# Optimization experiments

Measured on AMD Instinct MI355X. Metric: run time of the kernel, lower is better.

The kernel has to match this reference:

```python
import jax, jax.numpy as jnp
import numpy as np

B, T, D = 64, 4096, 512

def setup_inputs() -> dict:
    key = jax.random.key(0)
    k1, k2 = jax.random.split(key)
    encoder_outputs = jax.random.normal(k1, (B, T, D), dtype=jnp.float32)
    attn_weights_param = jax.random.normal(k2, (D, 1), dtype=jnp.float32)
    return {"encoder_outputs": encoder_outputs, "attn_weights_param": attn_weights_param}

def reference(encoder_outputs, attn_weights_param):
    # scores: [B, T] = encoder_outputs @ v  (GEMV per batch)
    energies = jnp.einsum('btd,d->bt', encoder_outputs, attn_weights_param[:, 0])
    weights = jax.nn.softmax(energies, axis=1)                 # [B, T]
    context = jnp.einsum('bt,btd->bd', weights, encoder_outputs)  # weighted-sum pool
    return (context, weights)
```

## Files before the change

### kernel.cpp

```cpp
#include <hip/hip_runtime.h>

constexpr int B = 64;
constexpr int T = 4096;
constexpr int D = 512;
constexpr int CHUNKS = 16;
constexpr int ROWS_PER_CHUNK = T / CHUNKS;
constexpr int PART_STRIDE = D + 2;

__device__ __forceinline__ float dot8(const float4& a0, const float4& v0,
                                      const float4& a1, const float4& v1) {
    return a0.x * v0.x + a0.y * v0.y + a0.z * v0.z + a0.w * v0.w
         + a1.x * v1.x + a1.y * v1.y + a1.z * v1.z + a1.w * v1.w;
}

__global__ __launch_bounds__(256) void attn_pass1(
    const float* __restrict__ enc,
    const float* __restrict__ v,
    float* __restrict__ energies,
    float* __restrict__ partials)
{
    const int blk   = blockIdx.x;
    const int b     = blk / CHUNKS;
    const int chunk = blk % CHUNKS;
    const int tid   = threadIdx.x;
    const int wave  = tid >> 6;
    const int lane  = tid & 63;

    const float4 v0 = *(const float4*)(v + lane * 4);
    const float4 v1 = *(const float4*)(v + 256 + lane * 4);

    float  m = -3.0e38f;
    float  l = 0.0f;
    float4 o0 = make_float4(0.f, 0.f, 0.f, 0.f);
    float4 o1 = make_float4(0.f, 0.f, 0.f, 0.f);

    const int t0 = chunk * ROWS_PER_CHUNK;
    const float* encb = enc + (size_t)b * T * D;

    for (int k = 0; k < ROWS_PER_CHUNK / 16; ++k) {
        const int t = t0 + k * 16 + wave * 4;
        const float* row = encb + (size_t)t * D;

        float4 a0[4], a1[4];
        #pragma unroll
        for (int r = 0; r < 4; ++r) {
            a0[r] = *(const float4*)(row + r * D + lane * 4);
            a1[r] = *(const float4*)(row + r * D + 256 + lane * 4);
        }

        float e[4];
        #pragma unroll
        for (int r = 0; r < 4; ++r)
            e[r] = dot8(a0[r], v0, a1[r], v1);

        #pragma unroll
        for (int off = 32; off > 0; off >>= 1) {
            #pragma unroll
            for (int r = 0; r < 4; ++r)
                e[r] += __shfl_xor(e[r], off, 64);
        }

        if (lane == 0)
            *(float4*)(energies + (size_t)b * T + t) =
                make_float4(e[0], e[1], e[2], e[3]);

        float m_new = m;
        #pragma unroll
        for (int r = 0; r < 4; ++r) m_new = fmaxf(m_new, e[r]);
        const float corr = __expf(m - m_new);
        float p[4];
        #pragma unroll
        for (int r = 0; r < 4; ++r) p[r] = __expf(e[r] - m_new);
        l = l * corr + p[0] + p[1] + p[2] + p[3];

        o0.x = o0.x * corr + p[0]*a0[0].x + p[1]*a0[1].x + p[2]*a0[2].x + p[3]*a0[3].x;
        o0.y = o0.y * corr + p[0]*a0[0].y + p[1]*a0[1].y + p[2]*a0[2].y + p[3]*a0[3].y;
        o0.z = o0.z * corr + p[0]*a0[0].z + p[1]*a0[1].z + p[2]*a0[2].z + p[3]*a0[3].z;
        o0.w = o0.w * corr + p[0]*a0[0].w + p[1]*a0[1].w + p[2]*a0[2].w + p[3]*a0[3].w;
        o1.x = o1.x * corr + p[0]*a1[0].x + p[1]*a1[1].x + p[2]*a1[2].x + p[3]*a1[3].x;
        o1.y = o1.y * corr + p[0]*a1[0].y + p[1]*a1[1].y + p[2]*a1[2].y + p[3]*a1[3].y;
        o1.z = o1.z * corr + p[0]*a1[0].z + p[1]*a1[1].z + p[2]*a1[2].z + p[3]*a1[3].z;
        o1.w = o1.w * corr + p[0]*a1[0].w + p[1]*a1[1].w + p[2]*a1[2].w + p[3]*a1[3].w;
        m = m_new;
    }

    __shared__ float sm[4];
    __shared__ float sl[4];
    __shared__ float so[4][D];

    if (lane == 0) { sm[wave] = m; sl[wave] = l; }
    *(float4*)&so[wave][lane * 4]       = o0;
    *(float4*)&so[wave][256 + lane * 4] = o1;
    __syncthreads();

    const float m_blk = fmaxf(fmaxf(sm[0], sm[1]), fmaxf(sm[2], sm[3]));
    const float s0 = __expf(sm[0] - m_blk);
    const float s1 = __expf(sm[1] - m_blk);
    const float s2 = __expf(sm[2] - m_blk);
    const float s3 = __expf(sm[3] - m_blk);
    const float l_blk = sl[0] * s0 + sl[1] * s1 + sl[2] * s2 + sl[3] * s3;

    float* part = partials + (size_t)blk * PART_STRIDE;
    if (tid == 0) { part[0] = m_blk; part[1] = l_blk; }
    for (int d = tid; d < D; d += 256) {
        part[2 + d] = so[0][d] * s0 + so[1][d] * s1
                    + so[2][d] * s2 + so[3][d] * s3;
    }
}

__global__ __launch_bounds__(256) void attn_pass2(
    const float* __restrict__ partials,
    float* __restrict__ ctx,
    float* __restrict__ weights)
{
    const int b     = blockIdx.x >> 2;
    const int slice = blockIdx.x & 3;
    const int tid   = threadIdx.x;
    const float* pb = partials + (size_t)b * CHUNKS * PART_STRIDE;

    float m_g = -3.0e38f;
    #pragma unroll
    for (int c = 0; c < CHUNKS; ++c)
        m_g = fmaxf(m_g, pb[c * PART_STRIDE]);

    float sc[CHUNKS];
    float l_g = 0.0f;
    #pragma unroll
    for (int c = 0; c < CHUNKS; ++c) {
        const float s = __expf(pb[c * PART_STRIDE] - m_g);
        sc[c] = s;
        l_g += pb[c * PART_STRIDE + 1] * s;
    }
    const float inv_l = 1.0f / l_g;

    if (slice == 0) {
        for (int d = tid; d < D; d += 256) {
            float acc = 0.0f;
            #pragma unroll
            for (int c = 0; c < CHUNKS; ++c)
                acc += pb[c * PART_STRIDE + 2 + d] * sc[c];
            ctx[(size_t)b * D + d] = acc * inv_l;
        }
    }

    float* wrow = weights + (size_t)b * T + slice * (T / 4);
    float4 w = *(float4*)(wrow + tid * 4);
    w.x = __expf(w.x - m_g) * inv_l;
    w.y = __expf(w.y - m_g) * inv_l;
    w.z = __expf(w.z - m_g) * inv_l;
    w.w = __expf(w.w - m_g) * inv_l;
    *(float4*)(wrow + tid * 4) = w;
}

extern "C" void kernel_launch(void* const* d_in, const int* in_sizes, int n_in,
                              void* d_out, int out_size, void* d_ws, size_t ws_size,
                              hipStream_t stream) {
    const float* enc = (const float*)d_in[0];
    const float* v   = (const float*)d_in[1];
    float* out     = (float*)d_out;
    float* ctx     = out;
    float* weights = out + B * D;
    float* partials = (float*)d_ws;

    attn_pass1<<<B * CHUNKS, 256, 0, stream>>>(enc, v, weights, partials);
    attn_pass2<<<B * 4, 256, 0, stream>>>(partials, ctx, weights);
}
```

Before: 680.1 us.

## Double-buffer row loads and use lazy rescaling in online softmax pass

Restructures the pass-1 loop to prefetch the next 16-row group into a second register buffer while the current group is reduced. It also replaces the per-step softmax rescale with a thresholded lazy rescale and skips accumulation for row groups far below the running max. It adds a minimum occupancy hint to launch bounds. The aim is to hide global load latency and cut exp/multiply work, at the cost of more registers and tiny numerical approximation for skipped rows.

```diff
diff --git a/kernel.cpp b/kernel.cpp
--- a/kernel.cpp
+++ b/kernel.cpp
@@ -13,7 +13,7 @@
          + a1.x * v1.x + a1.y * v1.y + a1.z * v1.z + a1.w * v1.w;
 }
 
-__global__ __launch_bounds__(256) void attn_pass1(
+__global__ __launch_bounds__(256, 4) void attn_pass1(
     const float* __restrict__ enc,
     const float* __restrict__ v,
     float* __restrict__ energies,
@@ -37,52 +37,69 @@
     const int t0 = chunk * ROWS_PER_CHUNK;
     const float* encb = enc + (size_t)b * T * D;
 
-    for (int k = 0; k < ROWS_PER_CHUNK / 16; ++k) {
-        const int t = t0 + k * 16 + wave * 4;
-        const float* row = encb + (size_t)t * D;
+    float4 A0[4], A1[4], B0[4], B1[4];
 
-        float4 a0[4], a1[4];
-        #pragma unroll
-        for (int r = 0; r < 4; ++r) {
-            a0[r] = *(const float4*)(row + r * D + lane * 4);
-            a1[r] = *(const float4*)(row + r * D + 256 + lane * 4);
-        }
+#define LOADROWS(buf0, buf1, kk) do {                                          \
+    const float* _row = encb + (size_t)(t0 + (kk) * 16 + wave * 4) * D         \
+                        + lane * 4;                                            \
+    _Pragma("unroll")                                                          \
+    for (int _r = 0; _r < 4; ++_r) {                                           \
+        buf0[_r] = *(const float4*)(_row + _r * D);                            \
+        buf1[_r] = *(const float4*)(_row + _r * D + 256);                      \
+    }                                                                          \
+} while (0)
 
-        float e[4];
-        #pragma unroll
-        for (int r = 0; r < 4; ++r)
-            e[r] = dot8(a0[r], v0, a1[r], v1);
+#define PROCESS(buf0, buf1, kk) do {                                           \
+    float e[4];                                                                \
+    _Pragma("unroll")                                                          \
+    for (int _r = 0; _r < 4; ++_r)                                             \
+        e[_r] = dot8(buf0[_r], v0, buf1[_r], v1);                              \
+                         \
+    _Pragma("unroll")                                                          \
+    for (int _off = 32; _off > 0; _off >>= 1) {                                \
+        _Pragma("unroll")                                                      \
+        for (int _r = 0; _r < 4; ++_r)                                         \
+            e[_r] += __shfl_xor(e[_r], _off, 64);                              \
+    }                                                                          \
+    if (lane == 0)                                                             \
+        *(float4*)(energies + (size_t)b * T + (t0 + (kk) * 16 + wave * 4)) =   \
+            make_float4(e[0], e[1], e[2], e[3]);                               \
+    const float emax = fmaxf(fmaxf(e[0], e[1]), fmaxf(e[2], e[3]));            \
+                   \
+    if (emax > m + 10.0f) {                                                    \
+        const float _corr = __expf(m - emax);                                  \
+        l *= _corr;                                                            \
+        o0.x *= _corr; o0.y *= _corr; o0.z *= _corr; o0.w *= _corr;            \
+        o1.x *= _corr; o1.y *= _corr; o1.z *= _corr; o1.w *= _corr;            \
+        m = emax;                                                              \
+    }                                                                          \
+                  \
+    if (emax >= m - 25.0f) {                                                   \
+        float p[4];                                                            \
+        _Pragma("unroll")                                                      \
+        for (int _r = 0; _r < 4; ++_r) p[_r] = __expf(e[_r] - m);              \
+        l += p[0] + p[1] + p[2] + p[3];                                        \
+        o0.x += p[0]*buf0[0].x + p[1]*buf0[1].x + p[2]*buf0[2].x + p[3]*buf0[3].x; \
+        o0.y += p[0]*buf0[0].y + p[1]*buf0[1].y + p[2]*buf0[2].y + p[3]*buf0[3].y; \
+        o0.z += p[0]*buf0[0].z + p[1]*buf0[1].z + p[2]*buf0[2].z + p[3]*buf0[3].z; \
+        o0.w += p[0]*buf0[0].w + p[1]*buf0[1].w + p[2]*buf0[2].w + p[3]*buf0[3].w; \
+        o1.x += p[0]*buf1[0].x + p[1]*buf1[1].x + p[2]*buf1[2].x + p[3]*buf1[3].x; \
+        o1.y += p[0]*buf1[0].y + p[1]*buf1[1].y + p[2]*buf1[2].y + p[3]*buf1[3].y; \
+        o1.z += p[0]*buf1[0].z + p[1]*buf1[1].z + p[2]*buf1[2].z + p[3]*buf1[3].z; \
+        o1.w += p[0]*buf1[0].w + p[1]*buf1[1].w + p[2]*buf1[2].w + p[3]*buf1[3].w; \
+    }                                                                          \
+} while (0)
 
-        #pragma unroll
-        for (int off = 32; off > 0; off >>= 1) {
-            #pragma unroll
-            for (int r = 0; r < 4; ++r)
-                e[r] += __shfl_xor(e[r], off, 64);
-        }
+    LOADROWS(A0, A1, 0);
+    for (int j = 0; j < 8; ++j) {
+        LOADROWS(B0, B1, 2 * j + 1);
+        PROCESS(A0, A1, 2 * j);
+        if (j < 7) LOADROWS(A0, A1, 2 * j + 2);
+        PROCESS(B0, B1, 2 * j + 1);
+    }
 
-        if (lane == 0)
-            *(float4*)(energies + (size_t)b * T + t) =
-                make_float4(e[0], e[1], e[2], e[3]);
-
-        float m_new = m;
-        #pragma unroll
-        for (int r = 0; r < 4; ++r) m_new = fmaxf(m_new, e[r]);
-        const float corr = __expf(m - m_new);
-        float p[4];
-        #pragma unroll
-        for (int r = 0; r < 4; ++r) p[r] = __expf(e[r] - m_new);
-        l = l * corr + p[0] + p[1] + p[2] + p[3];
-
-        o0.x = o0.x * corr + p[0]*a0[0].x + p[1]*a0[1].x + p[2]*a0[2].x + p[3]*a0[3].x;
-        o0.y = o0.y * corr + p[0]*a0[0].y + p[1]*a0[1].y + p[2]*a0[2].y + p[3]*a0[3].y;
-        o0.z = o0.z * corr + p[0]*a0[0].z + p[1]*a0[1].z + p[2]*a0[2].z + p[3]*a0[3].z;
-        o0.w = o0.w * corr + p[0]*a0[0].w + p[1]*a0[1].w + p[2]*a0[2].w + p[3]*a0[3].w;
-        o1.x = o1.x * corr + p[0]*a1[0].x + p[1]*a1[1].x + p[2]*a1[2].x + p[3]*a1[3].x;
-        o1.y = o1.y * corr + p[0]*a1[0].y + p[1]*a1[1].y + p[2]*a1[2].y + p[3]*a1[3].y;
-        o1.z = o1.z * corr + p[0]*a1[0].z + p[1]*a1[1].z + p[2]*a1[2].z + p[3]*a1[3].z;
-        o1.w = o1.w * corr + p[0]*a1[0].w + p[1]*a1[1].w + p[2]*a1[2].w + p[3]*a1[3].w;
-        m = m_new;
-    }
+#undef LOADROWS
+#undef PROCESS
 
     __shared__ float sm[4];
     __shared__ float sl[4];
```

After: 679.9 us. Within noise of the previous version (-0.0%).
